# Performance work log

Hardware: AMD Instinct MI355X
Metric: run time of the kernel (lower is better)

## Reference

```python
import jax, jax.numpy as jnp
import numpy as np

TOP_K = 2          # n_activated_experts
ROUTE_SCALE = 1.0  # args.route_scale


def setup_inputs() -> dict:
    key = jax.random.key(0)
    ks = jax.random.split(key, 12)
    B, S, D, I, E = 8, 2048, 512, 1024, 8
    SH = 2 * I  # n_shared_experts * moe_inter_dim
    std = 0.02
    return {
        "x": jax.random.normal(ks[0], (B, S, D), jnp.float32),
        "gate_w": (jax.random.normal(ks[1], (E, D), jnp.float32) * std),
        "w1": (jax.random.normal(ks[2], (E, D, I), jnp.float32) * std),
        "w2": (jax.random.normal(ks[3], (E, I, D), jnp.float32) * std),
        "w3": (jax.random.normal(ks[4], (E, D, I), jnp.float32) * std),
        "sw1": (jax.random.normal(ks[5], (D, SH), jnp.float32) * std),
        "sb1": jnp.zeros((SH,), jnp.float32),
        "sw2": (jax.random.normal(ks[6], (SH, D), jnp.float32) * std),
        "sb2": jnp.zeros((D,), jnp.float32),
        "sw3": (jax.random.normal(ks[7], (D, SH), jnp.float32) * std),
        "sb3": jnp.zeros((SH,), jnp.float32),
    }


def reference(x, gate_w, w1, w2, w3, sw1, sb1, sw2, sb2, sw3, sb3):
    B, S, D = x.shape
    xt = x.reshape(-1, D)              # [T, D] tokens
    T = xt.shape[0]
    E = gate_w.shape[0]

    # --- Gate: sigmoid scores, top-k, renormalized weights ---
    scores = jax.nn.sigmoid(xt @ gate_w.T)                 # [T, E]
    topv, topi = jax.lax.top_k(scores, TOP_K)              # [T, K]
    wts = topv / jnp.sum(topv, axis=-1, keepdims=True)
    wts = wts * ROUTE_SCALE

    # Dense combine weights: zero for non-selected experts -> faithful to
    # the torch masked scatter-accumulate over the expert loop.
    cw = jnp.zeros((T, E), xt.dtype).at[jnp.arange(T)[:, None], topi].add(wts)

    # --- Routed SwiGLU experts (ffn_bias=False) ---
    y = jnp.zeros_like(xt)
    for e in range(E):  # fixed small structural loop over experts
        h = jax.nn.silu(xt @ w1[e]) * (xt @ w3[e])         # [T, I]
        y = y + cw[:, e:e + 1] * (h @ w2[e])               # combine

    # --- Load-balance aux loss L_ExpBal ---
    counts = jnp.zeros((E,), xt.dtype).at[topi.reshape(-1)].add(1.0)
    f_i = E * counts / (TOP_K * T)
    P_i = cw.sum(axis=0) / T   # per-expert sum of routed weights
    L_ExpBal = jnp.sum(f_i * P_i)

    # --- Shared experts MLP (biased Linear, SwiGLU) ---
    z = (jax.nn.silu(xt @ sw1 + sb1) * (xt @ sw3 + sb3)) @ sw2 + sb2

    return (y + z).reshape(B, S, D), L_ExpBal
```

## Files before the change

kernel.cpp:

```cpp
#include <hip/hip_runtime.h>
#include <math.h>
#include <stdint.h>

#define T_TOK 16384
#define DDIM  512
#define IDIM  1024
#define NEXP  8
#define SHDIM 2048
#define MT_R  264
#define MPAD  (MT_R * 128)
#define GBLK  256

typedef unsigned short u16;
typedef short bf16x8 __attribute__((ext_vector_type(8)));
typedef float f32x4 __attribute__((ext_vector_type(4)));

__device__ __forceinline__ u16 f2bf(float f) {
    unsigned u = __float_as_uint(f);
    u += 0x7FFF + ((u >> 16) & 1);
    return (u16)(u >> 16);
}
__device__ __forceinline__ float bf2f(u16 h) {
    return __uint_as_float((unsigned)h << 16);
}

__device__ __forceinline__ void gload_lds16(const void* g, void* l) {
    __builtin_amdgcn_global_load_lds(
        (const __attribute__((address_space(1))) void*)g,
        (__attribute__((address_space(3))) void*)l, 16, 0, 0);
}

__device__ __forceinline__ int xcd_swz(int id, int nwg) {
    return (id & 7) * (nwg >> 3) + (id >> 3);
}

__global__ void k_zero(int* cursors) {
    int i = threadIdx.x;
    if (i < NEXP) cursors[i] = 0;
}

__global__ __launch_bounds__(256) void k_gate(
    const float* __restrict__ x, const float* __restrict__ gw,
    int* __restrict__ topi, float* __restrict__ wts,
    int* __restrict__ pcnt, float* __restrict__ pps, u16* __restrict__ xb)
{
    __shared__ int   cnt[NEXP];
    __shared__ float ps[NEXP];
    const int tid = threadIdx.x;
    if (tid < NEXP) { cnt[tid] = 0; ps[tid] = 0.f; }
    __syncthreads();
    const int wid = tid >> 6, lane = tid & 63;

    const float4* gw4 = (const float4*)gw;
    float4 g0[NEXP], g1[NEXP];
#pragma unroll
    for (int e = 0; e < NEXP; e++) {
        g0[e] = gw4[e * 128 + lane];
        g1[e] = gw4[e * 128 + 64 + lane];
    }

    const int t0 = blockIdx.x * 64 + wid * 16;
    for (int u = 0; u < 16; u++) {
        int t = t0 + u;
        const float4* xr4 = (const float4*)(x + (size_t)t * DDIM);
        float4 v0 = xr4[lane];
        float4 v1 = xr4[64 + lane];
        ushort4 o0 = { f2bf(v0.x), f2bf(v0.y), f2bf(v0.z), f2bf(v0.w) };
        ushort4 o1 = { f2bf(v1.x), f2bf(v1.y), f2bf(v1.z), f2bf(v1.w) };
        ushort4* xbo = (ushort4*)(xb + (size_t)t * DDIM);
        xbo[lane] = o0;
        xbo[64 + lane] = o1;
        float acc[NEXP];
#pragma unroll
        for (int e = 0; e < NEXP; e++) {
            acc[e] = v0.x * g0[e].x + v0.y * g0[e].y + v0.z * g0[e].z + v0.w * g0[e].w
                   + v1.x * g1[e].x + v1.y * g1[e].y + v1.z * g1[e].z + v1.w * g1[e].w;
        }
#pragma unroll
        for (int e = 0; e < NEXP; e++) {
#pragma unroll
            for (int off = 32; off; off >>= 1) acc[e] += __shfl_xor(acc[e], off, 64);
        }
        if (lane == 0) {
            float s[NEXP];
#pragma unroll
            for (int e = 0; e < NEXP; e++) s[e] = 1.f / (1.f + expf(-acc[e]));
            int i1 = 0; float v1s = s[0];
#pragma unroll
            for (int e = 1; e < NEXP; e++) if (s[e] > v1s) { v1s = s[e]; i1 = e; }
            int i2 = -1; float v2s = -1.f;
#pragma unroll
            for (int e = 0; e < NEXP; e++) if (e != i1 && s[e] > v2s) { v2s = s[e]; i2 = e; }
            float inv = 1.f / (v1s + v2s);
            float wa = v1s * inv, wb = v2s * inv;
            topi[2 * t] = i1; topi[2 * t + 1] = i2;
            wts[2 * t] = wa;  wts[2 * t + 1] = wb;
            atomicAdd(&cnt[i1], 1); atomicAdd(&cnt[i2], 1);
            atomicAdd(&ps[i1], wa); atomicAdd(&ps[i2], wb);
        }
    }
    __syncthreads();
    if (tid < NEXP) {
        pcnt[blockIdx.x * NEXP + tid] = cnt[tid];
        pps[blockIdx.x * NEXP + tid]  = ps[tid];
    }
}

__global__ void k_scan(const int* __restrict__ pcnt, const float* __restrict__ pps,
                       int* __restrict__ off_pad, float* __restrict__ out_loss)
{
    __shared__ int   scnt[8][NEXP];
    __shared__ float sps[8][NEXP];
    int tid = threadIdx.x;
    if (tid < 64) {
        int e = tid & 7, part = tid >> 3;
        int c = 0; float p = 0.f;
        for (int b = part * 32; b < part * 32 + 32; b++) {
            c += pcnt[b * NEXP + e];
            p += pps[b * NEXP + e];
        }
        scnt[part][e] = c; sps[part][e] = p;
    }
    __syncthreads();
    if (tid == 0) {
        int off = 0; float L = 0.f;
        for (int e = 0; e < NEXP; e++) {
            int c = 0; float p = 0.f;
            for (int q = 0; q < 8; q++) { c += scnt[q][e]; p += sps[q][e]; }
            off_pad[e] = off;
            off += (c + 127) & ~127;
            float f = (float)NEXP * (float)c / (float)(2 * T_TOK);
            L += f * (p / (float)T_TOK);
        }
        off_pad[NEXP] = off;
        out_loss[0] = L;
    }
}

__global__ void k_fillperm(int* __restrict__ perm) {
    int i = blockIdx.x * blockDim.x + threadIdx.x;
    if (i < MPAD) perm[i] = -1;
}

__global__ __launch_bounds__(256) void k_scatter(
    const int* __restrict__ topi, const float* __restrict__ wts,
    const int* __restrict__ off_pad, int* __restrict__ cursors,
    int* __restrict__ perm, float* __restrict__ pw, int* __restrict__ inv)
{
    __shared__ int lcnt[NEXP];
    __shared__ int lbase[NEXP];
    int tid = threadIdx.x;
    if (tid < NEXP) lcnt[tid] = 0;
    __syncthreads();
    int t = blockIdx.x * 256 + tid;
    int e0 = topi[2 * t], e1 = topi[2 * t + 1];
    int p0 = atomicAdd(&lcnt[e0], 1);
    int p1 = atomicAdd(&lcnt[e1], 1);
    __syncthreads();
    if (tid < NEXP) lbase[tid] = atomicAdd(&cursors[tid], lcnt[tid]);
    __syncthreads();
    int s0 = off_pad[e0] + lbase[e0] + p0;
    int s1 = off_pad[e1] + lbase[e1] + p1;
    perm[s0] = t; pw[s0] = wts[2 * t];
    perm[s1] = t; pw[s1] = wts[2 * t + 1];
    inv[2 * t] = s0; inv[2 * t + 1] = s1;
}

__global__ __launch_bounds__(256) void k_gather(const u16* __restrict__ xb,
                                                const int* __restrict__ perm,
                                                u16* __restrict__ xg) {
    int row = blockIdx.x * 2 + (threadIdx.x >> 7);
    int c = (threadIdx.x & 127) * 4;
    int tok = perm[row];
    ushort4 v = {0, 0, 0, 0};
    if (tok >= 0) v = *(const ushort4*)&xb[(size_t)tok * DDIM + c];
    *(ushort4*)&xg[(size_t)row * DDIM + c] = v;
}

__global__ __launch_bounds__(256) void k_transpose(const float* __restrict__ src,
                                                   u16* __restrict__ dst, int R, int C)
{
    __shared__ u16 t[64][68];
    const float* s = src + (size_t)blockIdx.z * R * C;
    u16* d = dst + (size_t)blockIdx.z * R * C;
    int r0 = blockIdx.y * 64, c0 = blockIdx.x * 64;
    int tid = threadIdx.x;
    int lr = tid >> 4, lc = (tid & 15) * 4;
#pragma unroll
    for (int u = 0; u < 4; u++) {
        int r = lr + u * 16;
        float4 v = *(const float4*)&s[(size_t)(r0 + r) * C + c0 + lc];
        t[lc + 0][r] = f2bf(v.x);
        t[lc + 1][r] = f2bf(v.y);
        t[lc + 2][r] = f2bf(v.z);
        t[lc + 3][r] = f2bf(v.w);
    }
    __syncthreads();
    int wr = tid >> 4, wc = (tid & 15) * 4;
#pragma unroll
    for (int u = 0; u < 4; u++) {
        int c = wr + u * 16;
        ushort4 o = { t[c][wc], t[c][wc + 1], t[c][wc + 2], t[c][wc + 3] };
        *(ushort4*)&d[(size_t)(c0 + c) * R + r0 + wc] = o;
    }
}

template<int K, bool ROUTED, bool BIAS>
__global__ __launch_bounds__(256, 2) void k_s1(
    const u16* __restrict__ A, const u16* __restrict__ B1t, const u16* __restrict__ B3t,
    const float* __restrict__ bias1, const float* __restrict__ bias3,
    u16* __restrict__ H, int ldh, const int* __restrict__ off_pad)
{
    __shared__ __align__(16) u16 sA[2][128 * 32], sB1[2][128 * 32], sB3[2][128 * 32];
    const int nwg = gridDim.x * gridDim.y;
    const int id  = xcd_swz(blockIdx.y * gridDim.x + blockIdx.x, nwg);
    const int m0 = (id / gridDim.x) * 128;
    const int n0 = (id % gridDim.x) * 128;
    if (ROUTED && m0 >= off_pad[NEXP]) return;
    const u16* b1 = B1t; const u16* b3 = B3t;
    if (ROUTED) {
        int e = 0;
        while (off_pad[e + 1] <= m0) e++;
        b1 += (size_t)e * IDIM * DDIM;
        b3 += (size_t)e * IDIM * DDIM;
    }
    const int tid = threadIdx.x;
    const int wid = tid >> 6, lane = tid & 63;
    const int srow = wid * 16 + (lane >> 2);
    const int skk  = (lane & 3) * 8;
    const u16* gA  = A  + (size_t)(m0 + srow) * K + skk;
    const u16* gB1 = b1 + (size_t)(n0 + srow) * K + skk;
    const u16* gB3 = b3 + (size_t)(n0 + srow) * K + skk;
    const int ldst = wid * 512;
    const int fr = lane & 15;
    const int fk = (lane >> 4) * 8;
    const int wrow = (wid >> 1) * 64, wcol = (wid & 1) * 64;

    f32x4 acc1[4][4], acc3[4][4];
#pragma unroll
    for (int i = 0; i < 4; i++)
#pragma unroll
        for (int j = 0; j < 4; j++) { acc1[i][j] = {0.f, 0.f, 0.f, 0.f}; acc3[i][j] = {0.f, 0.f, 0.f, 0.f}; }

#pragma unroll
    for (int p = 0; p < 2; p++) {
        gload_lds16(gA  + (size_t)p * 64 * K, &sA [0][ldst + p * 2048]);
        gload_lds16(gB1 + (size_t)p * 64 * K, &sB1[0][ldst + p * 2048]);
        gload_lds16(gB3 + (size_t)p * 64 * K, &sB3[0][ldst + p * 2048]);
    }
    __syncthreads();

    int cur = 0;
    for (int k0 = 0; k0 < K; k0 += 32) {
        if (k0 + 32 < K) {
#pragma unroll
            for (int p = 0; p < 2; p++) {
                gload_lds16(gA  + (size_t)p * 64 * K + k0 + 32, &sA [cur ^ 1][ldst + p * 2048]);
                gload_lds16(gB1 + (size_t)p * 64 * K + k0 + 32, &sB1[cur ^ 1][ldst + p * 2048]);
                gload_lds16(gB3 + (size_t)p * 64 * K + k0 + 32, &sB3[cur ^ 1][ldst + p * 2048]);
            }
        }
        bf16x8 av[4], b1v[4], b3v[4];
#pragma unroll
        for (int i = 0; i < 4; i++) {
            av[i]  = *(const bf16x8*)(&sA [cur][(wrow + i * 16 + fr) * 32 + fk]);
            b1v[i] = *(const bf16x8*)(&sB1[cur][(wcol + i * 16 + fr) * 32 + fk]);
            b3v[i] = *(const bf16x8*)(&sB3[cur][(wcol + i * 16 + fr) * 32 + fk]);
        }
#pragma unroll
        for (int i = 0; i < 4; i++)
#pragma unroll
            for (int j = 0; j < 4; j++) {
                acc1[i][j] = __builtin_amdgcn_mfma_f32_16x16x32_bf16(av[i], b1v[j], acc1[i][j], 0, 0, 0);
                acc3[i][j] = __builtin_amdgcn_mfma_f32_16x16x32_bf16(av[i], b3v[j], acc3[i][j], 0, 0, 0);
            }
        __syncthreads();
        cur ^= 1;
    }

    const int rr = (lane >> 4) * 4;
#pragma unroll
    for (int i = 0; i < 4; i++) {
#pragma unroll
        for (int j = 0; j < 4; j++) {
            int col = n0 + wcol + j * 16 + fr;
            float bb1 = BIAS ? bias1[col] : 0.f;
            float bb3 = BIAS ? bias3[col] : 0.f;
#pragma unroll
            for (int r = 0; r < 4; r++) {
                int row = m0 + wrow + i * 16 + rr + r;
                float v1 = acc1[i][j][r] + bb1;
                float v3 = acc3[i][j][r] + bb3;
                float hv = (v1 / (1.f + __expf(-v1))) * v3;
                H[(size_t)row * ldh + col] = f2bf(hv);
            }
        }
    }
}

template<int K, bool ROUTED>
__global__ __launch_bounds__(256, 2) void k_s2(
    const u16* __restrict__ A, const u16* __restrict__ Bt,
    const float* __restrict__ bias2, float* __restrict__ out,
    u16* __restrict__ ytmp, const int* __restrict__ off_pad)
{
    __shared__ __align__(16) u16 sA[2][128 * 32], sB[2][128 * 32];
    const int nwg = gridDim.x * gridDim.y;
    const int id  = xcd_swz(blockIdx.y * gridDim.x + blockIdx.x, nwg);
    const int m0 = (id / gridDim.x) * 128;
    const int n0 = (id % gridDim.x) * 128;
    if (ROUTED && m0 >= off_pad[NEXP]) return;
    const u16* bt = Bt;
    if (ROUTED) {
        int e = 0;
        while (off_pad[e + 1] <= m0) e++;
        bt += (size_t)e * DDIM * IDIM;
    }
    const int tid = threadIdx.x;
    const int wid = tid >> 6, lane = tid & 63;
    const int srow = wid * 16 + (lane >> 2);
    const int skk  = (lane & 3) * 8;
    const u16* gA = A  + (size_t)(m0 + srow) * K + skk;
    const u16* gB = bt + (size_t)(n0 + srow) * K + skk;
    const int ldst = wid * 512;
    const int fr = lane & 15;
    const int fk = (lane >> 4) * 8;
    const int wrow = (wid >> 1) * 64, wcol = (wid & 1) * 64;

    f32x4 acc[4][4];
#pragma unroll
    for (int i = 0; i < 4; i++)
#pragma unroll
        for (int j = 0; j < 4; j++) acc[i][j] = {0.f, 0.f, 0.f, 0.f};

#pragma unroll
    for (int p = 0; p < 2; p++) {
        gload_lds16(gA + (size_t)p * 64 * K, &sA[0][ldst + p * 2048]);
        gload_lds16(gB + (size_t)p * 64 * K, &sB[0][ldst + p * 2048]);
    }
    __syncthreads();

    int cur = 0;
    for (int k0 = 0; k0 < K; k0 += 32) {
        if (k0 + 32 < K) {
#pragma unroll
            for (int p = 0; p < 2; p++) {
                gload_lds16(gA + (size_t)p * 64 * K + k0 + 32, &sA[cur ^ 1][ldst + p * 2048]);
                gload_lds16(gB + (size_t)p * 64 * K + k0 + 32, &sB[cur ^ 1][ldst + p * 2048]);
            }
        }
        bf16x8 av[4], bv[4];
#pragma unroll
        for (int i = 0; i < 4; i++) {
            av[i] = *(const bf16x8*)(&sA[cur][(wrow + i * 16 + fr) * 32 + fk]);
            bv[i] = *(const bf16x8*)(&sB[cur][(wcol + i * 16 + fr) * 32 + fk]);
        }
#pragma unroll
        for (int i = 0; i < 4; i++)
#pragma unroll
            for (int j = 0; j < 4; j++)
                acc[i][j] = __builtin_amdgcn_mfma_f32_16x16x32_bf16(av[i], bv[j], acc[i][j], 0, 0, 0);
        __syncthreads();
        cur ^= 1;
    }

    const int rr = (lane >> 4) * 4;
#pragma unroll
    for (int i = 0; i < 4; i++) {
#pragma unroll
        for (int r = 0; r < 4; r++) {
            int row = m0 + wrow + i * 16 + rr + r;
#pragma unroll
            for (int j = 0; j < 4; j++) {
                int col = n0 + wcol + j * 16 + fr;
                float v = acc[i][j][r];
                if (ROUTED) {
                    ytmp[(size_t)row * DDIM + col] = f2bf(v);
                } else {
                    out[(size_t)row * DDIM + col] = v + bias2[col];
                }
            }
        }
    }
}

__global__ __launch_bounds__(256) void k_combine(
    const u16* __restrict__ ytmp, const int* __restrict__ inv,
    const float* __restrict__ wts, float* __restrict__ out)
{
    int idx = blockIdx.x * 256 + threadIdx.x;
    int t = idx >> 7;
    int c = (idx & 127) * 4;
    int s0 = inv[2 * t], s1 = inv[2 * t + 1];
    float w0 = wts[2 * t], w1 = wts[2 * t + 1];
    ushort4 a = *(const ushort4*)&ytmp[(size_t)s0 * DDIM + c];
    ushort4 b = *(const ushort4*)&ytmp[(size_t)s1 * DDIM + c];
    float4 o = *(float4*)&out[(size_t)t * DDIM + c];
    o.x += w0 * bf2f(a.x) + w1 * bf2f(b.x);
    o.y += w0 * bf2f(a.y) + w1 * bf2f(b.y);
    o.z += w0 * bf2f(a.z) + w1 * bf2f(b.z);
    o.w += w0 * bf2f(a.w) + w1 * bf2f(b.w);
    *(float4*)&out[(size_t)t * DDIM + c] = o;
}

extern "C" void kernel_launch(void* const* d_in, const int* in_sizes, int n_in,
                              void* d_out, int out_size, void* d_ws, size_t ws_size,
                              hipStream_t stream)
{
    const float* x   = (const float*)d_in[0];
    const float* gw  = (const float*)d_in[1];
    const float* w1  = (const float*)d_in[2];
    const float* w2  = (const float*)d_in[3];
    const float* w3  = (const float*)d_in[4];
    const float* sw1 = (const float*)d_in[5];
    const float* sb1 = (const float*)d_in[6];
    const float* sw2 = (const float*)d_in[7];
    const float* sb2 = (const float*)d_in[8];
    const float* sw3 = (const float*)d_in[9];
    const float* sb3 = (const float*)d_in[10];
    float* out = (float*)d_out;

    char* ws = (char*)d_ws;
    size_t off = 0;
    int*   topi    = (int*)(ws + off);   off += (size_t)2 * T_TOK * 4;
    float* wts     = (float*)(ws + off); off += (size_t)2 * T_TOK * 4;
    int*   perm    = (int*)(ws + off);   off += (size_t)MPAD * 4;
    float* pw      = (float*)(ws + off); off += (size_t)MPAD * 4;
    int*   cursors = (int*)(ws + off);   off += 256;
    int*   off_pad = (int*)(ws + off);   off += 256;
    int*   pcnt    = (int*)(ws + off);   off += (size_t)GBLK * NEXP * 4;
    float* pps     = (float*)(ws + off); off += (size_t)GBLK * NEXP * 4;
    int*   inv     = (int*)(ws + off);   off += (size_t)2 * T_TOK * 4;
    u16*   xb      = (u16*)(ws + off);   off += (size_t)T_TOK * DDIM * 2;
    u16*   xg      = (u16*)(ws + off);   off += (size_t)MPAD * DDIM * 2;
    u16*   w1T     = (u16*)(ws + off);   off += (size_t)NEXP * IDIM * DDIM * 2;
    u16*   w3T     = (u16*)(ws + off);   off += (size_t)NEXP * IDIM * DDIM * 2;
    u16*   w2T     = (u16*)(ws + off);   off += (size_t)NEXP * DDIM * IDIM * 2;
    u16*   sw1T    = (u16*)(ws + off);   off += (size_t)SHDIM * DDIM * 2;
    u16*   sw3T    = (u16*)(ws + off);   off += (size_t)SHDIM * DDIM * 2;
    u16*   sw2T    = (u16*)(ws + off);   off += (size_t)DDIM * SHDIM * 2;
    u16*   hb      = (u16*)(ws + off);   off += (size_t)MPAD * IDIM * 2;
    u16*   ytmp    = xg;

    k_zero<<<1, 64, 0, stream>>>(cursors);
    k_gate<<<GBLK, 256, 0, stream>>>(x, gw, topi, wts, pcnt, pps, xb);
    k_scan<<<1, 64, 0, stream>>>(pcnt, pps, off_pad, out + (size_t)T_TOK * DDIM);
    k_fillperm<<<(MPAD + 255) / 256, 256, 0, stream>>>(perm);
    k_scatter<<<T_TOK / 256, 256, 0, stream>>>(topi, wts, off_pad, cursors, perm, pw, inv);

    k_gather<<<MPAD / 2, 256, 0, stream>>>(xb, perm, xg);
    k_transpose<<<dim3(IDIM / 64, DDIM / 64, NEXP), 256, 0, stream>>>(w1, w1T, DDIM, IDIM);
    k_transpose<<<dim3(IDIM / 64, DDIM / 64, NEXP), 256, 0, stream>>>(w3, w3T, DDIM, IDIM);
    k_transpose<<<dim3(DDIM / 64, IDIM / 64, NEXP), 256, 0, stream>>>(w2, w2T, IDIM, DDIM);
    k_transpose<<<dim3(SHDIM / 64, DDIM / 64, 1), 256, 0, stream>>>(sw1, sw1T, DDIM, SHDIM);
    k_transpose<<<dim3(SHDIM / 64, DDIM / 64, 1), 256, 0, stream>>>(sw3, sw3T, DDIM, SHDIM);
    k_transpose<<<dim3(DDIM / 64, SHDIM / 64, 1), 256, 0, stream>>>(sw2, sw2T, SHDIM, DDIM);

    k_s1<DDIM, false, true><<<dim3(SHDIM / 128, T_TOK / 128), 256, 0, stream>>>(
        xb, sw1T, sw3T, sb1, sb3, hb, SHDIM, nullptr);
    k_s2<SHDIM, false><<<dim3(DDIM / 128, T_TOK / 128), 256, 0, stream>>>(
        hb, sw2T, sb2, out, nullptr, nullptr);
    k_s1<DDIM, true, false><<<dim3(IDIM / 128, MT_R), 256, 0, stream>>>(
        xg, w1T, w3T, nullptr, nullptr, hb, IDIM, off_pad);
    k_s2<IDIM, true><<<dim3(DDIM / 128, MT_R), 256, 0, stream>>>(
        hb, w2T, nullptr, nullptr, ytmp, off_pad);
    k_combine<<<(T_TOK * DDIM / 4) / 256, 256, 0, stream>>>(ytmp, inv, wts, out);
}
```

Measured before the change: 387.2 us.

## Interleave w1/w3 weights and use 256x256 tiles with swizzled LDS in SwiGLU GEMM

The transpose kernels now write w1 and w3 (and sw1/sw3) interleaved in 128-row blocks, so one B matrix feeds a single GEMM that computes both gate and up projections. k_s1 moves to 512 threads, 256x256 tiles, K-step 64, XOR-swizzled LDS, split A/B prefetch with explicit vmcnt waits and setprio. The w3 half of the accumulators is exchanged through LDS for the SwiGLU epilogue. Expert padding grows to 256 rows, which adds wasted rows in the routed GEMMs and uses 128KB of LDS per block, which may limit occupancy.

Result: slower. 464.4 us (+19.9%).

```diff
diff --git a/kernel.cpp b/kernel.cpp
--- a/kernel.cpp
+++ b/kernel.cpp
@@ -7,8 +7,7 @@
 #define IDIM  1024
 #define NEXP  8
 #define SHDIM 2048
-#define MT_R  264
-#define MPAD  (MT_R * 128)
+#define MPAD  34816
 #define GBLK  256
 
 typedef unsigned short u16;
@@ -128,7 +127,7 @@
             int c = 0; float p = 0.f;
             for (int q = 0; q < 8; q++) { c += scnt[q][e]; p += sps[q][e]; }
             off_pad[e] = off;
-            off += (c + 127) & ~127;
+            off += (c + 255) & ~255;
             float f = (float)NEXP * (float)c / (float)(2 * T_TOK);
             L += f * (p / (float)T_TOK);
         }
@@ -178,11 +177,12 @@
 }
 
 __global__ __launch_bounds__(256) void k_transpose(const float* __restrict__ src,
-                                                   u16* __restrict__ dst, int R, int C)
+                                                   u16* __restrict__ dst, int R, int C,
+                                                   int rmul, int radd, int zrows)
 {
     __shared__ u16 t[64][68];
     const float* s = src + (size_t)blockIdx.z * R * C;
-    u16* d = dst + (size_t)blockIdx.z * R * C;
+    u16* d = dst + (size_t)blockIdx.z * zrows * R;
     int r0 = blockIdx.y * 64, c0 = blockIdx.x * 64;
     int tid = threadIdx.x;
     int lr = tid >> 4, lc = (tid & 15) * 4;
@@ -200,101 +200,165 @@
 #pragma unroll
     for (int u = 0; u < 4; u++) {
         int c = wr + u * 16;
+        int gc = c0 + c;
+        int rp = (gc >> 7) * rmul + (gc & 127) + radd;
         ushort4 o = { t[c][wc], t[c][wc + 1], t[c][wc + 2], t[c][wc + 3] };
-        *(ushort4*)&d[(size_t)(c0 + c) * R + r0 + wc] = o;
-    }
-}
-
-template<int K, bool ROUTED, bool BIAS>
-__global__ __launch_bounds__(256, 2) void k_s1(
-    const u16* __restrict__ A, const u16* __restrict__ B1t, const u16* __restrict__ B3t,
+        *(ushort4*)&d[(size_t)rp * R + r0 + wc] = o;
+    }
+}
+
+template<bool ROUTED, bool BIAS, int NTX>
+__global__ __launch_bounds__(512, 2) void k_s1(
+    const u16* __restrict__ A, const u16* __restrict__ Bt,
     const float* __restrict__ bias1, const float* __restrict__ bias3,
     u16* __restrict__ H, int ldh, const int* __restrict__ off_pad)
 {
-    __shared__ __align__(16) u16 sA[2][128 * 32], sB1[2][128 * 32], sB3[2][128 * 32];
-    const int nwg = gridDim.x * gridDim.y;
-    const int id  = xcd_swz(blockIdx.y * gridDim.x + blockIdx.x, nwg);
-    const int m0 = (id / gridDim.x) * 128;
-    const int n0 = (id % gridDim.x) * 128;
+    __shared__ __align__(16) unsigned char smem[131072];
+    const int K = DDIM;
+    const int NT = K / 64;
+
+    const int nwg = NTX * gridDim.y;
+    int id = blockIdx.y * NTX + blockIdx.x;
+    id = xcd_swz(id, nwg);
+    const int mt = id / NTX, nt = id % NTX;
+    const int m0 = mt * 256;
     if (ROUTED && m0 >= off_pad[NEXP]) return;
-    const u16* b1 = B1t; const u16* b3 = B3t;
+    const u16* B = Bt;
     if (ROUTED) {
         int e = 0;
         while (off_pad[e + 1] <= m0) e++;
-        b1 += (size_t)e * IDIM * DDIM;
-        b3 += (size_t)e * IDIM * DDIM;
-    }
+        B += (size_t)e * (2 * IDIM) * DDIM;
+    }
+    const int n0r = nt * 256;
+
     const int tid = threadIdx.x;
     const int wid = tid >> 6, lane = tid & 63;
-    const int srow = wid * 16 + (lane >> 2);
-    const int skk  = (lane & 3) * 8;
-    const u16* gA  = A  + (size_t)(m0 + srow) * K + skk;
-    const u16* gB1 = b1 + (size_t)(n0 + srow) * K + skk;
-    const u16* gB3 = b3 + (size_t)(n0 + srow) * K + skk;
-    const int ldst = wid * 512;
-    const int fr = lane & 15;
-    const int fk = (lane >> 4) * 8;
-    const int wrow = (wid >> 1) * 64, wcol = (wid & 1) * 64;
-
-    f32x4 acc1[4][4], acc3[4][4];
-#pragma unroll
-    for (int i = 0; i < 4; i++)
-#pragma unroll
-        for (int j = 0; j < 4; j++) { acc1[i][j] = {0.f, 0.f, 0.f, 0.f}; acc3[i][j] = {0.f, 0.f, 0.f, 0.f}; }
-
-#pragma unroll
-    for (int p = 0; p < 2; p++) {
-        gload_lds16(gA  + (size_t)p * 64 * K, &sA [0][ldst + p * 2048]);
-        gload_lds16(gB1 + (size_t)p * 64 * K, &sB1[0][ldst + p * 2048]);
-        gload_lds16(gB3 + (size_t)p * 64 * K, &sB3[0][ldst + p * 2048]);
-    }
-    __syncthreads();
-
-    int cur = 0;
-    for (int k0 = 0; k0 < K; k0 += 32) {
-        if (k0 + 32 < K) {
-#pragma unroll
-            for (int p = 0; p < 2; p++) {
-                gload_lds16(gA  + (size_t)p * 64 * K + k0 + 32, &sA [cur ^ 1][ldst + p * 2048]);
-                gload_lds16(gB1 + (size_t)p * 64 * K + k0 + 32, &sB1[cur ^ 1][ldst + p * 2048]);
-                gload_lds16(gB3 + (size_t)p * 64 * K + k0 + 32, &sB3[cur ^ 1][ldst + p * 2048]);
-            }
-        }
-        bf16x8 av[4], b1v[4], b3v[4];
-#pragma unroll
-        for (int i = 0; i < 4; i++) {
-            av[i]  = *(const bf16x8*)(&sA [cur][(wrow + i * 16 + fr) * 32 + fk]);
-            b1v[i] = *(const bf16x8*)(&sB1[cur][(wcol + i * 16 + fr) * 32 + fk]);
-            b3v[i] = *(const bf16x8*)(&sB3[cur][(wcol + i * 16 + fr) * 32 + fk]);
-        }
-#pragma unroll
-        for (int i = 0; i < 4; i++)
+    const int wm = wid >> 2, wn = wid & 3;
+    const int fr = lane & 15, hi = lane >> 4;
+
+    int srow[4], sgo[4];
+#pragma unroll
+    for (int s = 0; s < 4; s++) {
+        int r = s * 64 + (tid >> 3);
+        srow[s] = r;
+        sgo[s] = ((tid & 7) ^ (r & 7)) * 8;
+    }
+    const int ldsw = wid * 1024;
+
+    f32x4 acc[8][4];
+#pragma unroll
+    for (int i = 0; i < 8; i++)
+#pragma unroll
+        for (int j = 0; j < 4; j++) acc[i][j] = {0.f, 0.f, 0.f, 0.f};
+
+#pragma unroll
+    for (int s = 0; s < 4; s++)
+        gload_lds16(A + (size_t)(m0 + srow[s]) * K + sgo[s], smem + s * 8192 + ldsw);
+#pragma unroll
+    for (int s = 0; s < 4; s++)
+        gload_lds16(B + (size_t)(n0r + srow[s]) * K + sgo[s], smem + 65536 + s * 8192 + ldsw);
+
+    const int ar0 = wm * 128;
+    const int br0 = wn * 64;
+
+    for (int t = 0; t < NT; t++) {
+        const int cur = (t & 1) << 15;
+        const int nxt = cur ^ 32768;
+        const int k0n = (t + 1) * 64;
+        if (t + 1 < NT) {
+#pragma unroll
+            for (int s = 0; s < 4; s++)
+                gload_lds16(A + (size_t)(m0 + srow[s]) * K + k0n + sgo[s],
+                            smem + nxt + s * 8192 + ldsw);
+            asm volatile("s_waitcnt vmcnt(4)" ::: "memory");
+        } else {
+            asm volatile("s_waitcnt vmcnt(0)" ::: "memory");
+        }
+        __builtin_amdgcn_s_barrier();
+        __builtin_amdgcn_sched_barrier(0);
+        {
+            bf16x8 av[8], bv[4];
 #pragma unroll
             for (int j = 0; j < 4; j++) {
-                acc1[i][j] = __builtin_amdgcn_mfma_f32_16x16x32_bf16(av[i], b1v[j], acc1[i][j], 0, 0, 0);
-                acc3[i][j] = __builtin_amdgcn_mfma_f32_16x16x32_bf16(av[i], b3v[j], acc3[i][j], 0, 0, 0);
-            }
-        __syncthreads();
-        cur ^= 1;
-    }
-
-    const int rr = (lane >> 4) * 4;
-#pragma unroll
-    for (int i = 0; i < 4; i++) {
-#pragma unroll
-        for (int j = 0; j < 4; j++) {
-            int col = n0 + wcol + j * 16 + fr;
-            float bb1 = BIAS ? bias1[col] : 0.f;
-            float bb3 = BIAS ? bias3[col] : 0.f;
-#pragma unroll
-            for (int r = 0; r < 4; r++) {
-                int row = m0 + wrow + i * 16 + rr + r;
-                float v1 = acc1[i][j][r] + bb1;
-                float v3 = acc3[i][j][r] + bb3;
-                float hv = (v1 / (1.f + __expf(-v1))) * v3;
-                H[(size_t)row * ldh + col] = f2bf(hv);
-            }
-        }
+                int br = br0 + j * 16 + fr;
+                bv[j] = *(const bf16x8*)(smem + 65536 + cur + br * 128 + (((hi) ^ (br & 7)) << 4));
+            }
+#pragma unroll
+            for (int i = 0; i < 8; i++) {
+                int ar = ar0 + i * 16 + fr;
+                av[i] = *(const bf16x8*)(smem + cur + ar * 128 + (((hi) ^ (ar & 7)) << 4));
+            }
+            __builtin_amdgcn_s_setprio(1);
+#pragma unroll
+            for (int i = 0; i < 8; i++)
+#pragma unroll
+                for (int j = 0; j < 4; j++)
+                    acc[i][j] = __builtin_amdgcn_mfma_f32_16x16x32_bf16(av[i], bv[j], acc[i][j], 0, 0, 0);
+            __builtin_amdgcn_s_setprio(0);
+        }
+        if (t + 1 < NT) {
+#pragma unroll
+            for (int s = 0; s < 4; s++)
+                gload_lds16(B + (size_t)(n0r + srow[s]) * K + k0n + sgo[s],
+                            smem + 65536 + nxt + s * 8192 + ldsw);
+        }
+        {
+            bf16x8 av[8], bv[4];
+#pragma unroll
+            for (int j = 0; j < 4; j++) {
+                int br = br0 + j * 16 + fr;
+                bv[j] = *(const bf16x8*)(smem + 65536 + cur + br * 128 + (((4 + hi) ^ (br & 7)) << 4));
+            }
+#pragma unroll
+            for (int i = 0; i < 8; i++) {
+                int ar = ar0 + i * 16 + fr;
+                av[i] = *(const bf16x8*)(smem + cur + ar * 128 + (((4 + hi) ^ (ar & 7)) << 4));
+            }
+            __builtin_amdgcn_s_setprio(1);
+#pragma unroll
+            for (int i = 0; i < 8; i++)
+#pragma unroll
+                for (int j = 0; j < 4; j++)
+                    acc[i][j] = __builtin_amdgcn_mfma_f32_16x16x32_bf16(av[i], bv[j], acc[i][j], 0, 0, 0);
+            __builtin_amdgcn_s_setprio(0);
+        }
+        __builtin_amdgcn_s_barrier();
+        __builtin_amdgcn_sched_barrier(0);
+    }
+
+    float* c3ex = (float*)smem;
+    if (wn >= 2) {
+#pragma unroll
+        for (int i = 0; i < 8; i++)
+#pragma unroll
+            for (int j = 0; j < 4; j++) {
+                int colb = (wn - 2) * 64 + j * 16 + fr;
+#pragma unroll
+                for (int r = 0; r < 4; r++) {
+                    int row = wm * 128 + i * 16 + hi * 4 + r;
+                    c3ex[row * 128 + colb] = acc[i][j][r];
+                }
+            }
+    }
+    __syncthreads();
+    if (wn < 2) {
+#pragma unroll
+        for (int i = 0; i < 8; i++)
+#pragma unroll
+            for (int j = 0; j < 4; j++) {
+                int colb = wn * 64 + j * 16 + fr;
+                int gcol = nt * 128 + colb;
+                float b1 = BIAS ? bias1[gcol] : 0.f;
+                float b3 = BIAS ? bias3[gcol] : 0.f;
+#pragma unroll
+                for (int r = 0; r < 4; r++) {
+                    int row = wm * 128 + i * 16 + hi * 4 + r;
+                    float v1 = acc[i][j][r] + b1;
+                    float v3 = c3ex[row * 128 + colb] + b3;
+                    float hv = (v1 / (1.f + __expf(-v1))) * v3;
+                    H[(size_t)(m0 + row) * ldh + gcol] = f2bf(hv);
+                }
+            }
     }
 }
 
@@ -433,11 +497,9 @@
     int*   inv     = (int*)(ws + off);   off += (size_t)2 * T_TOK * 4;
     u16*   xb      = (u16*)(ws + off);   off += (size_t)T_TOK * DDIM * 2;
     u16*   xg      = (u16*)(ws + off);   off += (size_t)MPAD * DDIM * 2;
-    u16*   w1T     = (u16*)(ws + off);   off += (size_t)NEXP * IDIM * DDIM * 2;
-    u16*   w3T     = (u16*)(ws + off);   off += (size_t)NEXP * IDIM * DDIM * 2;
+    u16*   w13Ts   = (u16*)(ws + off);   off += (size_t)2 * SHDIM * DDIM * 2;
+    u16*   w13Tr   = (u16*)(ws + off);   off += (size_t)NEXP * 2 * IDIM * DDIM * 2;
     u16*   w2T     = (u16*)(ws + off);   off += (size_t)NEXP * DDIM * IDIM * 2;
-    u16*   sw1T    = (u16*)(ws + off);   off += (size_t)SHDIM * DDIM * 2;
-    u16*   sw3T    = (u16*)(ws + off);   off += (size_t)SHDIM * DDIM * 2;
     u16*   sw2T    = (u16*)(ws + off);   off += (size_t)DDIM * SHDIM * 2;
     u16*   hb      = (u16*)(ws + off);   off += (size_t)MPAD * IDIM * 2;
     u16*   ytmp    = xg;
@@ -445,24 +507,24 @@
     k_zero<<<1, 64, 0, stream>>>(cursors);
     k_gate<<<GBLK, 256, 0, stream>>>(x, gw, topi, wts, pcnt, pps, xb);
     k_scan<<<1, 64, 0, stream>>>(pcnt, pps, off_pad, out + (size_t)T_TOK * DDIM);
-    k_fillperm<<<(MPAD + 255) / 256, 256, 0, stream>>>(perm);
+    k_fillperm<<<MPAD / 256, 256, 0, stream>>>(perm);
     k_scatter<<<T_TOK / 256, 256, 0, stream>>>(topi, wts, off_pad, cursors, perm, pw, inv);
-
     k_gather<<<MPAD / 2, 256, 0, stream>>>(xb, perm, xg);
-    k_transpose<<<dim3(IDIM / 64, DDIM / 64, NEXP), 256, 0, stream>>>(w1, w1T, DDIM, IDIM);
-    k_transpose<<<dim3(IDIM / 64, DDIM / 64, NEXP), 256, 0, stream>>>(w3, w3T, DDIM, IDIM);
-    k_transpose<<<dim3(DDIM / 64, IDIM / 64, NEXP), 256, 0, stream>>>(w2, w2T, IDIM, DDIM);
-    k_transpose<<<dim3(SHDIM / 64, DDIM / 64, 1), 256, 0, stream>>>(sw1, sw1T, DDIM, SHDIM);
-    k_transpose<<<dim3(SHDIM / 64, DDIM / 64, 1), 256, 0, stream>>>(sw3, sw3T, DDIM, SHDIM);
-    k_transpose<<<dim3(DDIM / 64, SHDIM / 64, 1), 256, 0, stream>>>(sw2, sw2T, SHDIM, DDIM);
-
-    k_s1<DDIM, false, true><<<dim3(SHDIM / 128, T_TOK / 128), 256, 0, stream>>>(
-        xb, sw1T, sw3T, sb1, sb3, hb, SHDIM, nullptr);
+
+    k_transpose<<<dim3(SHDIM / 64, DDIM / 64, 1), 256, 0, stream>>>(sw1, w13Ts, DDIM, SHDIM, 256, 0,   2 * SHDIM);
+    k_transpose<<<dim3(SHDIM / 64, DDIM / 64, 1), 256, 0, stream>>>(sw3, w13Ts, DDIM, SHDIM, 256, 128, 2 * SHDIM);
+    k_transpose<<<dim3(IDIM / 64, DDIM / 64, NEXP), 256, 0, stream>>>(w1, w13Tr, DDIM, IDIM, 256, 0,   2 * IDIM);
+    k_transpose<<<dim3(IDIM / 64, DDIM / 64, NEXP), 256, 0, stream>>>(w3, w13Tr, DDIM, IDIM, 256, 128, 2 * IDIM);
+    k_transpose<<<dim3(DDIM / 64, IDIM / 64, NEXP), 256, 0, stream>>>(w2, w2T, IDIM, DDIM, 128, 0, DDIM);
+    k_transpose<<<dim3(DDIM / 64, SHDIM / 64, 1), 256, 0, stream>>>(sw2, sw2T, SHDIM, DDIM, 128, 0, DDIM);
+
+    k_s1<false, true, 16><<<dim3(16, T_TOK / 256), 512, 0, stream>>>(
+        xb, w13Ts, sb1, sb3, hb, SHDIM, nullptr);
     k_s2<SHDIM, false><<<dim3(DDIM / 128, T_TOK / 128), 256, 0, stream>>>(
         hb, sw2T, sb2, out, nullptr, nullptr);
-    k_s1<DDIM, true, false><<<dim3(IDIM / 128, MT_R), 256, 0, stream>>>(
-        xg, w1T, w3T, nullptr, nullptr, hb, IDIM, off_pad);
-    k_s2<IDIM, true><<<dim3(DDIM / 128, MT_R), 256, 0, stream>>>(
+    k_s1<true, false, 8><<<dim3(8, MPAD / 256), 512, 0, stream>>>(
+        xg, w13Tr, nullptr, nullptr, hb, IDIM, off_pad);
+    k_s2<IDIM, true><<<dim3(DDIM / 128, MPAD / 128), 256, 0, stream>>>(
         hb, w2T, nullptr, nullptr, ytmp, off_pad);
     k_combine<<<(T_TOK * DDIM / 4) / 256, 256, 0, stream>>>(ytmp, inv, wts, out);
 }
```

## Fuse token gather into routed GEMM, triple-buffer LDS with XOR swizzle

Applied to the files above, without the earlier changes.

Drops the separate gather kernel: the routed stage-1 GEMM now reads token rows straight from xb through perm, with a zeroed pad row standing in for empty slots. Both GEMM kernels move from double to triple-buffered LDS, with explicit vmcnt waits, raw s_barrier, setprio around the MFMA block, and an XOR swizzle of K-chunks to cut LDS bank conflicts. k_s2 launch bounds rise to 3 waves per SIMD. The aim is to remove a full gather pass over memory and hide load latency better, at the cost of more LDS per block, hand-written waitcnt logic that must match the load counts exactly, and indirect row loads in the routed GEMM.

New measurement: 354.0 us. -8.6%, faster.

```diff
diff --git a/kernel.cpp b/kernel.cpp
--- a/kernel.cpp
+++ b/kernel.cpp
@@ -33,6 +33,8 @@
 __device__ __forceinline__ int xcd_swz(int id, int nwg) {
     return (id & 7) * (nwg >> 3) + (id >> 3);
 }
+
+__device__ __forceinline__ int ksw(int r) { return (r & 3) ^ ((r >> 2) & 3); }
 
 __global__ void k_zero(int* cursors) {
     int i = threadIdx.x;
@@ -137,9 +139,10 @@
     }
 }
 
-__global__ void k_fillperm(int* __restrict__ perm) {
+__global__ void k_fillperm(int* __restrict__ perm, u16* __restrict__ zpad) {
     int i = blockIdx.x * blockDim.x + threadIdx.x;
     if (i < MPAD) perm[i] = -1;
+    if (blockIdx.x == 0 && threadIdx.x < 256) ((unsigned*)zpad)[threadIdx.x] = 0u;
 }
 
 __global__ __launch_bounds__(256) void k_scatter(
@@ -164,17 +167,6 @@
     perm[s0] = t; pw[s0] = wts[2 * t];
     perm[s1] = t; pw[s1] = wts[2 * t + 1];
     inv[2 * t] = s0; inv[2 * t + 1] = s1;
-}
-
-__global__ __launch_bounds__(256) void k_gather(const u16* __restrict__ xb,
-                                                const int* __restrict__ perm,
-                                                u16* __restrict__ xg) {
-    int row = blockIdx.x * 2 + (threadIdx.x >> 7);
-    int c = (threadIdx.x & 127) * 4;
-    int tok = perm[row];
-    ushort4 v = {0, 0, 0, 0};
-    if (tok >= 0) v = *(const ushort4*)&xb[(size_t)tok * DDIM + c];
-    *(ushort4*)&xg[(size_t)row * DDIM + c] = v;
 }
 
 __global__ __launch_bounds__(256) void k_transpose(const float* __restrict__ src,
@@ -205,13 +197,14 @@
     }
 }
 
-template<int K, bool ROUTED, bool BIAS>
+template<bool ROUTED, bool BIAS>
 __global__ __launch_bounds__(256, 2) void k_s1(
-    const u16* __restrict__ A, const u16* __restrict__ B1t, const u16* __restrict__ B3t,
+    const u16* __restrict__ Axb, const u16* __restrict__ B1t, const u16* __restrict__ B3t,
     const float* __restrict__ bias1, const float* __restrict__ bias3,
-    u16* __restrict__ H, int ldh, const int* __restrict__ off_pad)
-{
-    __shared__ __align__(16) u16 sA[2][128 * 32], sB1[2][128 * 32], sB3[2][128 * 32];
+    u16* __restrict__ H, int ldh, const int* __restrict__ off_pad,
+    const int* __restrict__ perm, const u16* __restrict__ zpad)
+{
+    __shared__ __align__(16) unsigned char smem[3 * 24576];
     const int nwg = gridDim.x * gridDim.y;
     const int id  = xcd_swz(blockIdx.y * gridDim.x + blockIdx.x, nwg);
     const int m0 = (id / gridDim.x) * 128;
@@ -226,47 +219,81 @@
     }
     const int tid = threadIdx.x;
     const int wid = tid >> 6, lane = tid & 63;
-    const int srow = wid * 16 + (lane >> 2);
-    const int skk  = (lane & 3) * 8;
-    const u16* gA  = A  + (size_t)(m0 + srow) * K + skk;
-    const u16* gB1 = b1 + (size_t)(n0 + srow) * K + skk;
-    const u16* gB3 = b3 + (size_t)(n0 + srow) * K + skk;
-    const int ldst = wid * 512;
-    const int fr = lane & 15;
-    const int fk = (lane >> 4) * 8;
+    const int fr = lane & 15, hi = lane >> 4;
     const int wrow = (wid >> 1) * 64, wcol = (wid & 1) * 64;
 
+    const u16* ap[2]; const u16* b1p[2]; const u16* b3p[2];
+    int dst_[2];
+#pragma unroll
+    for (int s = 0; s < 2; s++) {
+        int r = s * 64 + (tid >> 2);
+        int goff = ((tid & 3) ^ ksw(r)) * 8;
+        dst_[s] = s * 4096 + tid * 16;
+        if (ROUTED) {
+            int tok = perm[m0 + r];
+            ap[s] = (tok >= 0 ? Axb + (size_t)tok * DDIM : zpad) + goff;
+        } else {
+            ap[s] = Axb + (size_t)(m0 + r) * DDIM + goff;
+        }
+        b1p[s] = b1 + (size_t)(n0 + r) * DDIM + goff;
+        b3p[s] = b3 + (size_t)(n0 + r) * DDIM + goff;
+    }
+    int aoff[4], boff[4];
+#pragma unroll
+    for (int i = 0; i < 4; i++) {
+        int ar = wrow + i * 16 + fr;
+        aoff[i] = ar * 64 + ((hi ^ ksw(ar)) << 4);
+        int br = wcol + i * 16 + fr;
+        boff[i] = br * 64 + ((hi ^ ksw(br)) << 4);
+    }
+
     f32x4 acc1[4][4], acc3[4][4];
 #pragma unroll
     for (int i = 0; i < 4; i++)
 #pragma unroll
         for (int j = 0; j < 4; j++) { acc1[i][j] = {0.f, 0.f, 0.f, 0.f}; acc3[i][j] = {0.f, 0.f, 0.f, 0.f}; }
 
-#pragma unroll
-    for (int p = 0; p < 2; p++) {
-        gload_lds16(gA  + (size_t)p * 64 * K, &sA [0][ldst + p * 2048]);
-        gload_lds16(gB1 + (size_t)p * 64 * K, &sB1[0][ldst + p * 2048]);
-        gload_lds16(gB3 + (size_t)p * 64 * K, &sB3[0][ldst + p * 2048]);
-    }
-    __syncthreads();
-
-    int cur = 0;
-    for (int k0 = 0; k0 < K; k0 += 32) {
-        if (k0 + 32 < K) {
-#pragma unroll
-            for (int p = 0; p < 2; p++) {
-                gload_lds16(gA  + (size_t)p * 64 * K + k0 + 32, &sA [cur ^ 1][ldst + p * 2048]);
-                gload_lds16(gB1 + (size_t)p * 64 * K + k0 + 32, &sB1[cur ^ 1][ldst + p * 2048]);
-                gload_lds16(gB3 + (size_t)p * 64 * K + k0 + 32, &sB3[cur ^ 1][ldst + p * 2048]);
+    const int NT = DDIM / 32;
+#pragma unroll
+    for (int t = 0; t < 2; t++) {
+        unsigned char* bb = smem + t * 24576;
+#pragma unroll
+        for (int s = 0; s < 2; s++) {
+            gload_lds16(ap[s]  + t * 32, bb + dst_[s]);
+            gload_lds16(b1p[s] + t * 32, bb + 8192  + dst_[s]);
+            gload_lds16(b3p[s] + t * 32, bb + 16384 + dst_[s]);
+        }
+    }
+
+    int bufc = 0;
+    for (int t = 0; t < NT; t++) {
+        int bufn = bufc + 2; if (bufn >= 3) bufn -= 3;
+        if (t + 2 < NT) {
+            unsigned char* bb = smem + bufn * 24576;
+            int k2 = (t + 2) * 32;
+#pragma unroll
+            for (int s = 0; s < 2; s++) {
+                gload_lds16(ap[s]  + k2, bb + dst_[s]);
+                gload_lds16(b1p[s] + k2, bb + 8192  + dst_[s]);
+                gload_lds16(b3p[s] + k2, bb + 16384 + dst_[s]);
             }
-        }
+            asm volatile("s_waitcnt vmcnt(12)" ::: "memory");
+        } else if (t + 2 == NT) {
+            asm volatile("s_waitcnt vmcnt(6)" ::: "memory");
+        } else {
+            asm volatile("s_waitcnt vmcnt(0)" ::: "memory");
+        }
+        __builtin_amdgcn_s_barrier();
+        __builtin_amdgcn_sched_barrier(0);
+        const unsigned char* cb = smem + bufc * 24576;
         bf16x8 av[4], b1v[4], b3v[4];
 #pragma unroll
         for (int i = 0; i < 4; i++) {
-            av[i]  = *(const bf16x8*)(&sA [cur][(wrow + i * 16 + fr) * 32 + fk]);
-            b1v[i] = *(const bf16x8*)(&sB1[cur][(wcol + i * 16 + fr) * 32 + fk]);
-            b3v[i] = *(const bf16x8*)(&sB3[cur][(wcol + i * 16 + fr) * 32 + fk]);
-        }
+            av[i]  = *(const bf16x8*)(cb + aoff[i]);
+            b1v[i] = *(const bf16x8*)(cb + 8192  + boff[i]);
+            b3v[i] = *(const bf16x8*)(cb + 16384 + boff[i]);
+        }
+        __builtin_amdgcn_s_setprio(1);
 #pragma unroll
         for (int i = 0; i < 4; i++)
 #pragma unroll
@@ -274,11 +301,13 @@
                 acc1[i][j] = __builtin_amdgcn_mfma_f32_16x16x32_bf16(av[i], b1v[j], acc1[i][j], 0, 0, 0);
                 acc3[i][j] = __builtin_amdgcn_mfma_f32_16x16x32_bf16(av[i], b3v[j], acc3[i][j], 0, 0, 0);
             }
-        __syncthreads();
-        cur ^= 1;
-    }
-
-    const int rr = (lane >> 4) * 4;
+        __builtin_amdgcn_s_setprio(0);
+        __builtin_amdgcn_sched_barrier(0);
+        __builtin_amdgcn_s_barrier();
+        bufc++; if (bufc >= 3) bufc -= 3;
+    }
+
+    const int rr = hi * 4;
 #pragma unroll
     for (int i = 0; i < 4; i++) {
 #pragma unroll
@@ -299,12 +328,12 @@
 }
 
 template<int K, bool ROUTED>
-__global__ __launch_bounds__(256, 2) void k_s2(
+__global__ __launch_bounds__(256, 3) void k_s2(
     const u16* __restrict__ A, const u16* __restrict__ Bt,
     const float* __restrict__ bias2, float* __restrict__ out,
     u16* __restrict__ ytmp, const int* __restrict__ off_pad)
 {
-    __shared__ __align__(16) u16 sA[2][128 * 32], sB[2][128 * 32];
+    __shared__ __align__(16) unsigned char smem[3 * 16384];
     const int nwg = gridDim.x * gridDim.y;
     const int id  = xcd_swz(blockIdx.y * gridDim.x + blockIdx.x, nwg);
     const int m0 = (id / gridDim.x) * 128;
@@ -318,53 +347,84 @@
     }
     const int tid = threadIdx.x;
     const int wid = tid >> 6, lane = tid & 63;
-    const int srow = wid * 16 + (lane >> 2);
-    const int skk  = (lane & 3) * 8;
-    const u16* gA = A  + (size_t)(m0 + srow) * K + skk;
-    const u16* gB = bt + (size_t)(n0 + srow) * K + skk;
-    const int ldst = wid * 512;
-    const int fr = lane & 15;
-    const int fk = (lane >> 4) * 8;
+    const int fr = lane & 15, hi = lane >> 4;
     const int wrow = (wid >> 1) * 64, wcol = (wid & 1) * 64;
 
+    const u16* ap[2]; const u16* bp[2];
+    int dst_[2];
+#pragma unroll
+    for (int s = 0; s < 2; s++) {
+        int r = s * 64 + (tid >> 2);
+        int goff = ((tid & 3) ^ ksw(r)) * 8;
+        dst_[s] = s * 4096 + tid * 16;
+        ap[s] = A  + (size_t)(m0 + r) * K + goff;
+        bp[s] = bt + (size_t)(n0 + r) * K + goff;
+    }
+    int aoff[4], boff[4];
+#pragma unroll
+    for (int i = 0; i < 4; i++) {
+        int ar = wrow + i * 16 + fr;
+        aoff[i] = ar * 64 + ((hi ^ ksw(ar)) << 4);
+        int br = wcol + i * 16 + fr;
+        boff[i] = br * 64 + ((hi ^ ksw(br)) << 4);
+    }
+
     f32x4 acc[4][4];
 #pragma unroll
     for (int i = 0; i < 4; i++)
 #pragma unroll
         for (int j = 0; j < 4; j++) acc[i][j] = {0.f, 0.f, 0.f, 0.f};
 
-#pragma unroll
-    for (int p = 0; p < 2; p++) {
-        gload_lds16(gA + (size_t)p * 64 * K, &sA[0][ldst + p * 2048]);
-        gload_lds16(gB + (size_t)p * 64 * K, &sB[0][ldst + p * 2048]);
-    }
-    __syncthreads();
-
-    int cur = 0;
-    for (int k0 = 0; k0 < K; k0 += 32) {
-        if (k0 + 32 < K) {
-#pragma unroll
-            for (int p = 0; p < 2; p++) {
-                gload_lds16(gA + (size_t)p * 64 * K + k0 + 32, &sA[cur ^ 1][ldst + p * 2048]);
-                gload_lds16(gB + (size_t)p * 64 * K + k0 + 32, &sB[cur ^ 1][ldst + p * 2048]);
+    const int NT = K / 32;
+#pragma unroll
+    for (int t = 0; t < 2; t++) {
+        unsigned char* bb = smem + t * 16384;
+#pragma unroll
+        for (int s = 0; s < 2; s++) {
+            gload_lds16(ap[s] + t * 32, bb + dst_[s]);
+            gload_lds16(bp[s] + t * 32, bb + 8192 + dst_[s]);
+        }
+    }
+
+    int bufc = 0;
+    for (int t = 0; t < NT; t++) {
+        int bufn = bufc + 2; if (bufn >= 3) bufn -= 3;
+        if (t + 2 < NT) {
+            unsigned char* bb = smem + bufn * 16384;
+            int k2 = (t + 2) * 32;
+#pragma unroll
+            for (int s = 0; s < 2; s++) {
+                gload_lds16(ap[s] + k2, bb + dst_[s]);
+                gload_lds16(bp[s] + k2, bb + 8192 + dst_[s]);
             }
-        }
+            asm volatile("s_waitcnt vmcnt(8)" ::: "memory");
+        } else if (t + 2 == NT) {
+            asm volatile("s_waitcnt vmcnt(4)" ::: "memory");
+        } else {
+            asm volatile("s_waitcnt vmcnt(0)" ::: "memory");
+        }
+        __builtin_amdgcn_s_barrier();
+        __builtin_amdgcn_sched_barrier(0);
+        const unsigned char* cb = smem + bufc * 16384;
         bf16x8 av[4], bv[4];
 #pragma unroll
         for (int i = 0; i < 4; i++) {
-            av[i] = *(const bf16x8*)(&sA[cur][(wrow + i * 16 + fr) * 32 + fk]);
-            bv[i] = *(const bf16x8*)(&sB[cur][(wcol + i * 16 + fr) * 32 + fk]);
-        }
+            av[i] = *(const bf16x8*)(cb + aoff[i]);
+            bv[i] = *(const bf16x8*)(cb + 8192 + boff[i]);
+        }
+        __builtin_amdgcn_s_setprio(1);
 #pragma unroll
         for (int i = 0; i < 4; i++)
 #pragma unroll
             for (int j = 0; j < 4; j++)
                 acc[i][j] = __builtin_amdgcn_mfma_f32_16x16x32_bf16(av[i], bv[j], acc[i][j], 0, 0, 0);
-        __syncthreads();
-        cur ^= 1;
-    }
-
-    const int rr = (lane >> 4) * 4;
+        __builtin_amdgcn_s_setprio(0);
+        __builtin_amdgcn_sched_barrier(0);
+        __builtin_amdgcn_s_barrier();
+        bufc++; if (bufc >= 3) bufc -= 3;
+    }
+
+    const int rr = hi * 4;
 #pragma unroll
     for (int i = 0; i < 4; i++) {
 #pragma unroll
@@ -431,8 +491,9 @@
     int*   pcnt    = (int*)(ws + off);   off += (size_t)GBLK * NEXP * 4;
     float* pps     = (float*)(ws + off); off += (size_t)GBLK * NEXP * 4;
     int*   inv     = (int*)(ws + off);   off += (size_t)2 * T_TOK * 4;
+    u16*   zpad    = (u16*)(ws + off);   off += 1024;
     u16*   xb      = (u16*)(ws + off);   off += (size_t)T_TOK * DDIM * 2;
-    u16*   xg      = (u16*)(ws + off);   off += (size_t)MPAD * DDIM * 2;
+    u16*   ytmp    = (u16*)(ws + off);   off += (size_t)MPAD * DDIM * 2;
     u16*   w1T     = (u16*)(ws + off);   off += (size_t)NEXP * IDIM * DDIM * 2;
     u16*   w3T     = (u16*)(ws + off);   off += (size_t)NEXP * IDIM * DDIM * 2;
     u16*   w2T     = (u16*)(ws + off);   off += (size_t)NEXP * DDIM * IDIM * 2;
@@ -440,15 +501,13 @@
     u16*   sw3T    = (u16*)(ws + off);   off += (size_t)SHDIM * DDIM * 2;
     u16*   sw2T    = (u16*)(ws + off);   off += (size_t)DDIM * SHDIM * 2;
     u16*   hb      = (u16*)(ws + off);   off += (size_t)MPAD * IDIM * 2;
-    u16*   ytmp    = xg;
 
     k_zero<<<1, 64, 0, stream>>>(cursors);
     k_gate<<<GBLK, 256, 0, stream>>>(x, gw, topi, wts, pcnt, pps, xb);
     k_scan<<<1, 64, 0, stream>>>(pcnt, pps, off_pad, out + (size_t)T_TOK * DDIM);
-    k_fillperm<<<(MPAD + 255) / 256, 256, 0, stream>>>(perm);
+    k_fillperm<<<MPAD / 256, 256, 0, stream>>>(perm, zpad);
     k_scatter<<<T_TOK / 256, 256, 0, stream>>>(topi, wts, off_pad, cursors, perm, pw, inv);
 
-    k_gather<<<MPAD / 2, 256, 0, stream>>>(xb, perm, xg);
     k_transpose<<<dim3(IDIM / 64, DDIM / 64, NEXP), 256, 0, stream>>>(w1, w1T, DDIM, IDIM);
     k_transpose<<<dim3(IDIM / 64, DDIM / 64, NEXP), 256, 0, stream>>>(w3, w3T, DDIM, IDIM);
     k_transpose<<<dim3(DDIM / 64, IDIM / 64, NEXP), 256, 0, stream>>>(w2, w2T, IDIM, DDIM);
@@ -456,12 +515,12 @@
     k_transpose<<<dim3(SHDIM / 64, DDIM / 64, 1), 256, 0, stream>>>(sw3, sw3T, DDIM, SHDIM);
     k_transpose<<<dim3(DDIM / 64, SHDIM / 64, 1), 256, 0, stream>>>(sw2, sw2T, SHDIM, DDIM);
 
-    k_s1<DDIM, false, true><<<dim3(SHDIM / 128, T_TOK / 128), 256, 0, stream>>>(
-        xb, sw1T, sw3T, sb1, sb3, hb, SHDIM, nullptr);
+    k_s1<false, true><<<dim3(SHDIM / 128, T_TOK / 128), 256, 0, stream>>>(
+        xb, sw1T, sw3T, sb1, sb3, hb, SHDIM, nullptr, nullptr, nullptr);
     k_s2<SHDIM, false><<<dim3(DDIM / 128, T_TOK / 128), 256, 0, stream>>>(
         hb, sw2T, sb2, out, nullptr, nullptr);
-    k_s1<DDIM, true, false><<<dim3(IDIM / 128, MT_R), 256, 0, stream>>>(
-        xg, w1T, w3T, nullptr, nullptr, hb, IDIM, off_pad);
+    k_s1<true, false><<<dim3(IDIM / 128, MT_R), 256, 0, stream>>>(
+        xb, w1T, w3T, nullptr, nullptr, hb, IDIM, off_pad, perm, zpad);
     k_s2<IDIM, true><<<dim3(DDIM / 128, MT_R), 256, 0, stream>>>(
         hb, w2T, nullptr, nullptr, ytmp, off_pad);
     k_combine<<<(T_TOK * DDIM / 4) / 256, 256, 0, stream>>>(ytmp, inv, wts, out);
```
